# Kernel optimization log

Measured on AMD Instinct MI355X. Metric: run time of the kernel, lower is better.

The kernel has to match this reference:

```python
import jax, jax.numpy as jnp
import numpy as np

DIM = 1024
NUM_HEADS = 16
HEAD_DIM = 64
EPS = 1e-6

def setup_inputs() -> dict:
    key = jax.random.key(0)
    ks = jax.random.split(key, 6)
    x = jax.random.normal(ks[0], (4, 2048, DIM), dtype=jnp.float32)
    # Linear weights stored as (in, out); torch nn.Linear computes x @ W.T with W (out,in),
    # equivalent math with our (in,out) layout.
    Wq = jax.random.normal(ks[1], (DIM, NUM_HEADS * HEAD_DIM), dtype=jnp.float32) / np.sqrt(DIM)
    Wk = jax.random.normal(ks[2], (DIM, NUM_HEADS * HEAD_DIM), dtype=jnp.float32) / np.sqrt(DIM)
    Wv = jax.random.normal(ks[3], (DIM, NUM_HEADS * HEAD_DIM), dtype=jnp.float32) / np.sqrt(DIM)
    Wo = jax.random.normal(ks[4], (NUM_HEADS * HEAD_DIM, DIM), dtype=jnp.float32) / np.sqrt(NUM_HEADS * HEAD_DIM)
    # FeatureMap buffer: randn(head_dim, head_dim)/sqrt(head_dim)
    proj = jax.random.normal(ks[5], (HEAD_DIM, HEAD_DIM), dtype=jnp.float32) / np.sqrt(HEAD_DIM)
    return {"x": x, "Wq": Wq, "Wk": Wk, "Wv": Wv, "Wo": Wo, "proj": proj}

def _feature_map(x, proj):
    # phi(x) = elu(x @ proj) + 1  (positive features)
    return jax.nn.elu(x @ proj) + 1.0

def reference(x, Wq, Wk, Wv, Wo, proj):
    B, S, _ = x.shape
    H, D = NUM_HEADS, HEAD_DIM
    q = (x @ Wq).reshape(B, S, H, D)
    k = (x @ Wk).reshape(B, S, H, D)
    v = (x @ Wv).reshape(B, S, H, D)
    q = _feature_map(q, proj)
    k = _feature_map(k, proj)
    # scan over time: carry kv_state (B,H,D,D) and k_state (B,H,D)
    q_t = jnp.moveaxis(q, 1, 0)  # (S,B,H,D)
    k_t = jnp.moveaxis(k, 1, 0)
    v_t = jnp.moveaxis(v, 1, 0)

    def step(carry, qkv):
        kv, ksum = carry
        qt, kt, vt = qkv  # each (B,H,D)
        kv = kv + kt[..., :, None] * vt[..., None, :]  # outer product k v^T
        ksum = ksum + kt
        num = jnp.einsum('bhd,bhde->bhe', qt, kv)
        den = jnp.einsum('bhd,bhd->bh', qt, ksum) + EPS
        return (kv, ksum), num / den[..., None]

    kv0 = jnp.zeros((B, H, D, D), dtype=x.dtype)
    ks0 = jnp.zeros((B, H, D), dtype=x.dtype)
    _, out = jax.lax.scan(step, (kv0, ks0), (q_t, k_t, v_t))
    out = jnp.moveaxis(out, 0, 1).reshape(B, S, H * D)  # (B,S,H*D)
    return out @ Wo
```

## Files before the change

### kernel.cpp

```cpp
#include <hip/hip_runtime.h>

typedef unsigned short u16;
typedef unsigned int   u32;
typedef short bfrag8 __attribute__((ext_vector_type(8)));
typedef float facc4  __attribute__((ext_vector_type(4)));

#define DIM    1024
#define NH     16
#define HD     64
#define BSZ    4
#define SEQ    2048
#define MROWS  (BSZ*SEQ)
#define CHUNK  64
#define NCHUNK (SEQ/CHUNK)
#define BH     (BSZ*NH)
#define TS     72
#define NT     16

__device__ __forceinline__ u16 f2bf(float f) {
  u32 u = __builtin_bit_cast(u32, f);
  u32 r = u + 0x7fffu + ((u >> 16) & 1u);
  return (u16)(r >> 16);
}
__device__ __forceinline__ float bf2f(u16 b) {
  return __builtin_bit_cast(float, (u32)b << 16);
}

__device__ __forceinline__ void gload_lds16(const void* g, void* l) {
  __builtin_amdgcn_global_load_lds((const __attribute__((address_space(1))) u32*)g,
                                   (__attribute__((address_space(3))) u32*)l, 16, 0, 0);
}


__global__ __launch_bounds__(256) void conv_f32_bf16(const float* __restrict__ in, u16* __restrict__ out) {
  const int i = (blockIdx.x * 256 + threadIdx.x) * 4;
  const float4 v = *(const float4*)(in + i);
  ushort4 o;
  o.x = f2bf(v.x); o.y = f2bf(v.y); o.z = f2bf(v.z); o.w = f2bf(v.w);
  *(ushort4*)(out + i) = o;
}

__global__ __launch_bounds__(256) void fold_qk(const float* __restrict__ Wq, const float* __restrict__ Wk,
                                               const float* __restrict__ proj, u16* __restrict__ wt) {
  const int i0 = blockIdx.x * 32;
  const int h  = blockIdx.y;
  const int sel = blockIdx.z;
  const float* W = sel ? Wk : Wq;
  u16* out = wt + (size_t)sel * (DIM*DIM);
  __shared__ float sp[64*64];
  __shared__ float sw[32*64];
  const int tid = threadIdx.x;
  for (int idx = tid; idx < 4096; idx += 256) sp[idx] = proj[idx];
  for (int idx = tid; idx < 2048; idx += 256) {
    int r = idx >> 6, c = idx & 63;
    sw[idx] = W[(size_t)(i0 + r)*DIM + h*64 + c];
  }
  __syncthreads();
  const int i  = tid >> 3;
  const int e0 = (tid & 7) * 8;
  #pragma unroll
  for (int ee = 0; ee < 8; ++ee) {
    const int e = e0 + ee;
    float acc = 0.f;
    for (int d = 0; d < 64; ++d) acc += sw[i*64 + d] * sp[d*64 + e];
    out[(size_t)(h*64 + e)*DIM + i0 + i] = f2bf(acc);
  }
}

__global__ __launch_bounds__(256) void trans_conv(const float* __restrict__ Wv, const float* __restrict__ Wo,
                                                  u16* __restrict__ wt) {
  const int sel = blockIdx.z;
  const float* in = sel ? Wo : Wv;
  u16* out = wt + (size_t)(2 + sel) * (DIM*DIM);
  const int n0 = blockIdx.x * 32, k0 = blockIdx.y * 32;
  __shared__ float tile[32][33];
  const int tid = threadIdx.x;
  for (int idx = tid; idx < 1024; idx += 256) {
    int r = idx >> 5, c = idx & 31;
    tile[r][c] = in[(size_t)(k0 + r)*DIM + n0 + c];
  }
  __syncthreads();
  for (int idx = tid; idx < 1024; idx += 256) {
    int r = idx >> 5, c = idx & 31;
    out[(size_t)(n0 + r)*DIM + k0 + c] = f2bf(tile[c][r]);
  }
}


#define SBAR0() __builtin_amdgcn_sched_barrier(0)

#define STAGE6(kt, bp) { \
  const int rih = tid >> 3, sl = tid & 7; \
  const int gc = ((sl ^ (rih & 7)) << 3); \
  _Pragma("unroll") for (int seg = 0; seg < 2; ++seg) \
    gload_lds16(A + (size_t)(m0 + seg*64 + rih)*DIM + (kt)*64 + gc, (bp) + seg*4096 + tid*8); \
  _Pragma("unroll") for (int seg = 0; seg < 4; ++seg) \
    gload_lds16(W + (size_t)(ngl + seg*64 + rih)*DIM + (kt)*64 + gc, (bp) + 8192 + seg*4096 + tid*8); \
}

#define RD8(xd, wd, bp, KH) { \
  _Pragma("unroll") for (int mf = 0; mf < 4; ++mf) { \
    const int row = wm*64 + mf*16 + lr; \
    xd[mf] = *(const bfrag8*)&(bp)[row*64 + ((((KH)*4+g) ^ (row & 7)) << 3)]; } \
  _Pragma("unroll") for (int nf = 0; nf < 4; ++nf) { \
    const int row = wn*64 + nf*16 + lr; \
    wd[nf] = *(const bfrag8*)&(bp)[8192 + row*64 + ((((KH)*4+g) ^ (row & 7)) << 3)]; } \
}

#define MM16(xs, ws) { __builtin_amdgcn_s_setprio(1); \
  _Pragma("unroll") for (int nf = 0; nf < 4; ++nf) \
    _Pragma("unroll") for (int mf = 0; mf < 4; ++mf) \
      acc[nf][mf] = __builtin_amdgcn_mfma_f32_16x16x32_bf16(ws[nf], xs[mf], acc[nf][mf], 0, 0, 0); \
  __builtin_amdgcn_s_setprio(0); }

template<int MODE>
__global__ __launch_bounds__(512, 1)
void gemmK(const u16* __restrict__ A, const u16* __restrict__ W,
           u16* __restrict__ outb, float* __restrict__ outf) {
  __shared__ u16 lds[2*24576];
  const int tid  = threadIdx.x;
  const int wave = tid >> 6, lane = tid & 63;
  const int wm = wave >> 2, wn = wave & 3;
  const int lr = lane & 15, g = lane >> 4;

  const int NY  = (MODE == 0) ? 12 : 4;
  const int q   = (int)gridDim.x >> 3;
  const int bid = (int)blockIdx.x;
  const int nf_ = (bid & 7) * q + (bid >> 3);
  const int m0  = (nf_ / NY) * 128;
  const int ngl = (nf_ % NY) * 256;

  STAGE6(0, lds);
  STAGE6(1, lds + 24576);
  asm volatile("s_waitcnt vmcnt(6)" ::: "memory");
  asm volatile("s_barrier" ::: "memory");

  facc4 acc[4][4] = {};
  bfrag8 xa[4], wa[4], xb[4], wb[4];

  RD8(xa, wa, lds, 0);

  #pragma unroll 2
  for (int t = 0; t < NT; ++t) {
    u16* bufp = lds + (t & 1) * 24576;
    u16* bufq = lds + ((t + 1) & 1) * 24576;
    asm volatile("s_waitcnt lgkmcnt(0)" ::: "memory"); SBAR0();
    RD8(xb, wb, bufp, 1);
    SBAR0();
    MM16(xa, wa);
    SBAR0();
    asm volatile("s_waitcnt vmcnt(0)" ::: "memory");
    asm volatile("s_barrier" ::: "memory");
    asm volatile("s_waitcnt lgkmcnt(0)" ::: "memory"); SBAR0();
    if (t + 2 < NT) STAGE6(t + 2, bufp);
    if (t + 1 < NT) RD8(xa, wa, bufq, 0);
    SBAR0();
    MM16(xb, wb);
    SBAR0();
    asm volatile("s_barrier" ::: "memory");
  }

  const int sel = (MODE == 0) ? (ngl >> 10) : 0;
  const bool doElu = (MODE == 0) && (sel < 2);
  const int coly = (MODE == 0) ? (ngl & 1023) : ngl;
  #pragma unroll
  for (int nf = 0; nf < 4; ++nf) {
    #pragma unroll
    for (int mf = 0; mf < 4; ++mf) {
      const facc4 a = acc[nf][mf];
      const int m = m0 + wm*64 + mf*16 + lr;
      const int col0 = coly + wn*64 + nf*16 + g*4;
      float v0 = a[0], v1 = a[1], v2 = a[2], v3 = a[3];
      if (MODE == 0) {
        if (doElu) {
          v0 = (v0 > 0.f) ? (v0 + 1.f) : __expf(v0);
          v1 = (v1 > 0.f) ? (v1 + 1.f) : __expf(v1);
          v2 = (v2 > 0.f) ? (v2 + 1.f) : __expf(v2);
          v3 = (v3 > 0.f) ? (v3 + 1.f) : __expf(v3);
        }
        uint2 pk;
        pk.x = (u32)f2bf(v0) | ((u32)f2bf(v1) << 16);
        pk.y = (u32)f2bf(v2) | ((u32)f2bf(v3) << 16);
        *(uint2*)&outb[(size_t)sel*((size_t)MROWS*DIM) + (size_t)m*DIM + col0] = pk;
      } else {
        float4 pk; pk.x = v0; pk.y = v1; pk.z = v2; pk.w = v3;
        *(float4*)&outf[(size_t)m*DIM + col0] = pk;
      }
    }
  }
}


__global__ __launch_bounds__(256) void phaseA(const u16* __restrict__ Kb, const u16* __restrict__ Vb,
                                              u16* __restrict__ Ast, float* __restrict__ ksum) {
  const int c = blockIdx.x, bh = blockIdx.y;
  const int b = bh >> 4, h = bh & 15;
  const int tid = threadIdx.x;
  const int wave = tid >> 6, lane = tid & 63, lr = lane & 15, g = lane >> 4;
  __shared__ u16 lKt[64*TS];
  __shared__ u16 lVt[64*TS];
  const size_t mbase = (size_t)b*SEQ + (size_t)c*CHUNK;

  for (int s = tid; s < 512; s += 256) {
    const int t = s >> 3, dg = (s & 7) * 8;
    const bfrag8 kk = *(const bfrag8*)&Kb[(mbase + t)*DIM + h*64 + dg];
    const bfrag8 vv = *(const bfrag8*)&Vb[(mbase + t)*DIM + h*64 + dg];
    #pragma unroll
    for (int j = 0; j < 8; ++j) {
      lKt[(dg + j)*TS + t] = (u16)kk[j];
      lVt[(dg + j)*TS + t] = (u16)vv[j];
    }
  }
  __syncthreads();

  facc4 acc[4] = {};
  #pragma unroll
  for (int kt = 0; kt < 2; ++kt) {
    const bfrag8 af = *(const bfrag8*)&lVt[(wave*16 + lr)*TS + kt*32 + g*8];
    #pragma unroll
    for (int j = 0; j < 4; ++j) {
      const bfrag8 bk = *(const bfrag8*)&lKt[(j*16 + lr)*TS + kt*32 + g*8];
      acc[j] = __builtin_amdgcn_mfma_f32_16x16x32_bf16(af, bk, acc[j], 0, 0, 0);
    }
  }
  u16* dst = Ast + (((size_t)bh*NCHUNK + c) << 12);
  #pragma unroll
  for (int j = 0; j < 4; ++j)
    #pragma unroll
    for (int r = 0; r < 4; ++r)
      dst[(wave*16 + g*4 + r)*64 + j*16 + lr] = f2bf(acc[j][r]);

  const int d = tid >> 2, seg = tid & 3;
  const bfrag8 k0 = *(const bfrag8*)&lKt[d*TS + seg*16];
  const bfrag8 k1 = *(const bfrag8*)&lKt[d*TS + seg*16 + 8];
  float s = 0.f;
  #pragma unroll
  for (int j = 0; j < 8; ++j) s += bf2f((u16)k0[j]) + bf2f((u16)k1[j]);
  s += __shfl_xor(s, 1, 64);
  s += __shfl_xor(s, 2, 64);
  if (seg == 0) ksum[((size_t)bh*NCHUNK + c)*64 + d] = s;
}

__global__ __launch_bounds__(256) void phaseB(u16* __restrict__ Ast, float* __restrict__ ksum) {
  const int bh = blockIdx.x, slice = blockIdx.y;
  const int tid = threadIdx.x;
  u16* base = Ast + (size_t)bh*NCHUNK*4096 + slice*256 + tid;
  float v[NCHUNK];
  #pragma unroll
  for (int c = 0; c < NCHUNK; ++c) v[c] = bf2f(base[(size_t)c*4096]);
  float run = 0.f;
  #pragma unroll
  for (int c = 0; c < NCHUNK; ++c) { base[(size_t)c*4096] = f2bf(run); run += v[c]; }
  if (slice == 0 && tid < 64) {
    float rs = 0.f;
    float* kp = ksum + (size_t)bh*NCHUNK*64 + tid;
    for (int c = 0; c < NCHUNK; ++c) { const float t = kp[c*64]; kp[c*64] = rs; rs += t; }
  }
}

__global__ __launch_bounds__(256) void phaseC(const u16* __restrict__ Qb, const u16* __restrict__ Kb,
                                              const u16* __restrict__ Vb, const u16* __restrict__ Ast,
                                              const float* __restrict__ ksum, u16* __restrict__ Ob) {
  const int c = blockIdx.x, bh = blockIdx.y;
  const int b = bh >> 4, h = bh & 15;
  const int tid = threadIdx.x;
  const int wave = tid >> 6, lane = tid & 63, lr = lane & 15, g = lane >> 4;
  __shared__ u16 lS  [64*TS];
  __shared__ u16 lVt [64*TS];
  __shared__ u16 lKVt[64*TS];
  __shared__ float lks[64];
  __shared__ float lrs[64];
  __shared__ float lqk[64];
  const size_t mbase = (size_t)b*SEQ + (size_t)c*CHUNK;

  for (int s = tid; s < 512; s += 256) {
    const int t = s >> 3, dg = (s & 7) * 8;
    const bfrag8 vv = *(const bfrag8*)&Vb[(mbase + t)*DIM + h*64 + dg];
    #pragma unroll
    for (int j = 0; j < 8; ++j) lVt[(dg + j)*TS + t] = (u16)vv[j];
  }
  const u16* kvsrc = Ast + (((size_t)bh*NCHUNK + c) << 12);
  for (int s = tid; s < 512; s += 256) {
    const int e = s >> 3, dg = (s & 7) * 8;
    *(bfrag8*)&lKVt[e*TS + dg] = *(const bfrag8*)&kvsrc[e*64 + dg];
  }
  if (tid < 64) lks[tid] = ksum[((size_t)bh*NCHUNK + c)*64 + tid];

  bfrag8 qf[2], kf[4][2];
  {
    const u16* qrow = Qb + (mbase + wave*16 + lr)*DIM + h*64;
    qf[0] = *(const bfrag8*)&qrow[g*8];
    qf[1] = *(const bfrag8*)&qrow[32 + g*8];
  }
  #pragma unroll
  for (int j = 0; j < 4; ++j) {
    const u16* krow = Kb + (mbase + j*16 + lr)*DIM + h*64;
    kf[j][0] = *(const bfrag8*)&krow[g*8];
    kf[j][1] = *(const bfrag8*)&krow[32 + g*8];
  }

  facc4 accs[4] = {};
  #pragma unroll
  for (int kt = 0; kt < 2; ++kt)
    #pragma unroll
    for (int j = 0; j < 4; ++j)
      accs[j] = __builtin_amdgcn_mfma_f32_16x16x32_bf16(qf[kt], kf[j][kt], accs[j], 0, 0, 0);

  float rs[4] = {0.f, 0.f, 0.f, 0.f};
  #pragma unroll
  for (int j = 0; j < 4; ++j) {
    const int cc = j*16 + lr;
    #pragma unroll
    for (int r = 0; r < 4; ++r) {
      const int rr = wave*16 + g*4 + r;
      const float vS = (cc <= rr) ? accs[j][r] : 0.f;
      rs[r] += vS;
      lS[rr*TS + cc] = f2bf(vS);
    }
  }
  #pragma unroll
  for (int r = 0; r < 4; ++r) {
    float t = rs[r];
    t += __shfl_xor(t, 1, 64); t += __shfl_xor(t, 2, 64);
    t += __shfl_xor(t, 4, 64); t += __shfl_xor(t, 8, 64);
    if (lr == 0) lrs[wave*16 + g*4 + r] = t;
  }
  __syncthreads();

  {
    const u16* qr2 = Qb + (mbase + wave*16 + lr)*DIM + h*64 + g*16;
    const bfrag8 a0 = *(const bfrag8*)&qr2[0];
    const bfrag8 a1 = *(const bfrag8*)&qr2[8];
    float t = 0.f;
    #pragma unroll
    for (int j = 0; j < 8; ++j)
      t += bf2f((u16)a0[j]) * lks[g*16 + j] + bf2f((u16)a1[j]) * lks[g*16 + 8 + j];
    t += __shfl_xor(t, 16, 64);
    t += __shfl_xor(t, 32, 64);
    if (g == 0) lqk[wave*16 + lr] = t;
  }

  facc4 acco[4] = {};
  #pragma unroll
  for (int kt = 0; kt < 2; ++kt) {
    const bfrag8 sf = *(const bfrag8*)&lS[(wave*16 + lr)*TS + kt*32 + g*8];
    #pragma unroll
    for (int j = 0; j < 4; ++j) {
      const bfrag8 vf = *(const bfrag8*)&lVt[(j*16 + lr)*TS + kt*32 + g*8];
      acco[j] = __builtin_amdgcn_mfma_f32_16x16x32_bf16(sf, vf, acco[j], 0, 0, 0);
    }
  }
  #pragma unroll
  for (int kt = 0; kt < 2; ++kt)
    #pragma unroll
    for (int j = 0; j < 4; ++j) {
      const bfrag8 kvf = *(const bfrag8*)&lKVt[(j*16 + lr)*TS + kt*32 + g*8];
      acco[j] = __builtin_amdgcn_mfma_f32_16x16x32_bf16(qf[kt], kvf, acco[j], 0, 0, 0);
    }

  #pragma unroll
  for (int r = 0; r < 4; ++r) {
    const int rr = wave*16 + g*4 + r;
    const float rden = 1.0f / (lrs[rr] + lqk[rr] + 1e-6f);
    #pragma unroll
    for (int j = 0; j < 4; ++j)
      Ob[(mbase + rr)*DIM + h*64 + j*16 + lr] = f2bf(acco[j][r] * rden);
  }
}

extern "C" void kernel_launch(void* const* d_in, const int* in_sizes, int n_in,
                              void* d_out, int out_size, void* d_ws, size_t ws_size,
                              hipStream_t stream) {
  const float* x    = (const float*)d_in[0];
  const float* Wq   = (const float*)d_in[1];
  const float* Wk   = (const float*)d_in[2];
  const float* Wv   = (const float*)d_in[3];
  const float* Wo   = (const float*)d_in[4];
  const float* proj = (const float*)d_in[5];
  float* out = (float*)d_out;

  char* ws = (char*)d_ws;
  u16*   xb   = (u16*)  (ws);
  u16*   wt   = (u16*)  (ws + 16777216);
  u16*   qkv  = (u16*)  (ws + 25165824);
  u16*   Ob   = (u16*)  (ws + 75497472);
  u16*   Ast  = (u16*)  (ws + 92274688);
  float* ksum = (float*)(ws + 109051904);
  (void)ws_size; (void)in_sizes; (void)n_in; (void)out_size;

  conv_f32_bf16<<<dim3((MROWS*DIM)/1024), 256, 0, stream>>>(x, xb);
  fold_qk      <<<dim3(DIM/32, NH, 2), 256, 0, stream>>>(Wq, Wk, proj, wt);
  trans_conv   <<<dim3(DIM/32, DIM/32, 2), 256, 0, stream>>>(Wv, Wo, wt);

  gemmK<0><<<dim3(64*12), 512, 0, stream>>>(xb, wt, qkv, nullptr);

  const u16* Qb = qkv;
  const u16* Kb = qkv + (size_t)MROWS*DIM;
  const u16* Vb = qkv + 2*(size_t)MROWS*DIM;

  phaseA<<<dim3(NCHUNK, BH), 256, 0, stream>>>(Kb, Vb, Ast, ksum);
  phaseB<<<dim3(BH, 16), 256, 0, stream>>>(Ast, ksum);
  phaseC<<<dim3(NCHUNK, BH), 256, 0, stream>>>(Qb, Kb, Vb, Ast, ksum, Ob);

  gemmK<1><<<dim3(64*4), 512, 0, stream>>>(Ob, wt + 3*(size_t)DIM*DIM, nullptr, out);
}
```

Baseline: 186.6 us.

## Merge prep kernels and fold chunk prefix sum into phaseC

```diff
diff --git a/kernel.cpp b/kernel.cpp
--- a/kernel.cpp
+++ b/kernel.cpp
@@ -31,61 +31,62 @@
                                    (__attribute__((address_space(3))) u32*)l, 16, 0, 0);
 }
 
-
-__global__ __launch_bounds__(256) void conv_f32_bf16(const float* __restrict__ in, u16* __restrict__ out) {
-  const int i = (blockIdx.x * 256 + threadIdx.x) * 4;
-  const float4 v = *(const float4*)(in + i);
-  ushort4 o;
-  o.x = f2bf(v.x); o.y = f2bf(v.y); o.z = f2bf(v.z); o.w = f2bf(v.w);
-  *(ushort4*)(out + i) = o;
-}
-
-__global__ __launch_bounds__(256) void fold_qk(const float* __restrict__ Wq, const float* __restrict__ Wk,
-                                               const float* __restrict__ proj, u16* __restrict__ wt) {
-  const int i0 = blockIdx.x * 32;
-  const int h  = blockIdx.y;
-  const int sel = blockIdx.z;
-  const float* W = sel ? Wk : Wq;
-  u16* out = wt + (size_t)sel * (DIM*DIM);
-  __shared__ float sp[64*64];
-  __shared__ float sw[32*64];
-  const int tid = threadIdx.x;
-  for (int idx = tid; idx < 4096; idx += 256) sp[idx] = proj[idx];
-  for (int idx = tid; idx < 2048; idx += 256) {
-    int r = idx >> 6, c = idx & 63;
-    sw[idx] = W[(size_t)(i0 + r)*DIM + h*64 + c];
-  }
-  __syncthreads();
-  const int i  = tid >> 3;
-  const int e0 = (tid & 7) * 8;
-  #pragma unroll
-  for (int ee = 0; ee < 8; ++ee) {
-    const int e = e0 + ee;
-    float acc = 0.f;
-    for (int d = 0; d < 64; ++d) acc += sw[i*64 + d] * sp[d*64 + e];
-    out[(size_t)(h*64 + e)*DIM + i0 + i] = f2bf(acc);
-  }
-}
-
-__global__ __launch_bounds__(256) void trans_conv(const float* __restrict__ Wv, const float* __restrict__ Wo,
-                                                  u16* __restrict__ wt) {
-  const int sel = blockIdx.z;
-  const float* in = sel ? Wo : Wv;
-  u16* out = wt + (size_t)(2 + sel) * (DIM*DIM);
-  const int n0 = blockIdx.x * 32, k0 = blockIdx.y * 32;
-  __shared__ float tile[32][33];
-  const int tid = threadIdx.x;
-  for (int idx = tid; idx < 1024; idx += 256) {
-    int r = idx >> 5, c = idx & 31;
-    tile[r][c] = in[(size_t)(k0 + r)*DIM + n0 + c];
-  }
-  __syncthreads();
-  for (int idx = tid; idx < 1024; idx += 256) {
-    int r = idx >> 5, c = idx & 31;
-    out[(size_t)(n0 + r)*DIM + k0 + c] = f2bf(tile[c][r]);
-  }
-}
-
+__global__ __launch_bounds__(256) void prep(const float* __restrict__ x,
+                                            const float* __restrict__ Wq, const float* __restrict__ Wk,
+                                            const float* __restrict__ Wv, const float* __restrict__ Wo,
+                                            const float* __restrict__ proj,
+                                            u16* __restrict__ xb, u16* __restrict__ wt) {
+  __shared__ float smem[6144];
+  const int bx = blockIdx.x, tid = threadIdx.x;
+  if (bx < 8192) {
+    const int i = (bx * 256 + tid) * 4;
+    const float4 v = *(const float4*)(x + i);
+    ushort4 o;
+    o.x = f2bf(v.x); o.y = f2bf(v.y); o.z = f2bf(v.z); o.w = f2bf(v.w);
+    *(ushort4*)(xb + i) = o;
+  } else if (bx < 9216) {
+    const int idx = bx - 8192;
+    const int i0 = (idx & 31) * 32;
+    const int h  = (idx >> 5) & 15;
+    const int sel = idx >> 9;
+    const float* W = sel ? Wk : Wq;
+    u16* out = wt + (size_t)sel * (DIM*DIM);
+    float* sp = smem;
+    float* sw = smem + 4096;
+    for (int s = tid; s < 4096; s += 256) sp[s] = proj[s];
+    for (int s = tid; s < 2048; s += 256) {
+      int r = s >> 6, c = s & 63;
+      sw[s] = W[(size_t)(i0 + r)*DIM + h*64 + c];
+    }
+    __syncthreads();
+    const int i  = tid >> 3;
+    const int e0 = (tid & 7) * 8;
+    #pragma unroll
+    for (int ee = 0; ee < 8; ++ee) {
+      const int e = e0 + ee;
+      float acc = 0.f;
+      for (int d = 0; d < 64; ++d) acc += sw[i*64 + d] * sp[d*64 + e];
+      out[(size_t)(h*64 + e)*DIM + i0 + i] = f2bf(acc);
+    }
+  } else {
+    const int idx = bx - 9216;
+    const int n0 = (idx & 31) * 32;
+    const int k0 = ((idx >> 5) & 31) * 32;
+    const int sel = idx >> 10;
+    const float* in = sel ? Wo : Wv;
+    u16* out = wt + (size_t)(2 + sel) * (DIM*DIM);
+    float* tile = smem;
+    for (int s = tid; s < 1024; s += 256) {
+      int r = s >> 5, c = s & 31;
+      tile[r*33 + c] = in[(size_t)(k0 + r)*DIM + n0 + c];
+    }
+    __syncthreads();
+    for (int s = tid; s < 1024; s += 256) {
+      int r = s >> 5, c = s & 31;
+      out[(size_t)(n0 + r)*DIM + k0 + c] = f2bf(tile[c*33 + r]);
+    }
+  }
+}
 
 #define SBAR0() __builtin_amdgcn_sched_barrier(0)
 
@@ -241,23 +242,6 @@
   if (seg == 0) ksum[((size_t)bh*NCHUNK + c)*64 + d] = s;
 }
 
-__global__ __launch_bounds__(256) void phaseB(u16* __restrict__ Ast, float* __restrict__ ksum) {
-  const int bh = blockIdx.x, slice = blockIdx.y;
-  const int tid = threadIdx.x;
-  u16* base = Ast + (size_t)bh*NCHUNK*4096 + slice*256 + tid;
-  float v[NCHUNK];
-  #pragma unroll
-  for (int c = 0; c < NCHUNK; ++c) v[c] = bf2f(base[(size_t)c*4096]);
-  float run = 0.f;
-  #pragma unroll
-  for (int c = 0; c < NCHUNK; ++c) { base[(size_t)c*4096] = f2bf(run); run += v[c]; }
-  if (slice == 0 && tid < 64) {
-    float rs = 0.f;
-    float* kp = ksum + (size_t)bh*NCHUNK*64 + tid;
-    for (int c = 0; c < NCHUNK; ++c) { const float t = kp[c*64]; kp[c*64] = rs; rs += t; }
-  }
-}
-
 __global__ __launch_bounds__(256) void phaseC(const u16* __restrict__ Qb, const u16* __restrict__ Kb,
                                               const u16* __restrict__ Vb, const u16* __restrict__ Ast,
                                               const float* __restrict__ ksum, u16* __restrict__ Ob) {
@@ -279,12 +263,28 @@
     #pragma unroll
     for (int j = 0; j < 8; ++j) lVt[(dg + j)*TS + t] = (u16)vv[j];
   }
-  const u16* kvsrc = Ast + (((size_t)bh*NCHUNK + c) << 12);
-  for (int s = tid; s < 512; s += 256) {
-    const int e = s >> 3, dg = (s & 7) * 8;
-    *(bfrag8*)&lKVt[e*TS + dg] = *(const bfrag8*)&kvsrc[e*64 + dg];
-  }
-  if (tid < 64) lks[tid] = ksum[((size_t)bh*NCHUNK + c)*64 + tid];
+  {
+    float pacc[16] = {};
+    const u16* abase = Ast + (((size_t)bh*NCHUNK) << 12) + tid*16;
+    for (int cc = 0; cc < c; ++cc) {
+      const bfrag8 a0 = *(const bfrag8*)&abase[(size_t)cc*4096];
+      const bfrag8 a1 = *(const bfrag8*)&abase[(size_t)cc*4096 + 8];
+      #pragma unroll
+      for (int jj = 0; jj < 8; ++jj) {
+        pacc[jj]     += bf2f((u16)a0[jj]);
+        pacc[8 + jj] += bf2f((u16)a1[jj]);
+      }
+    }
+    const int e = tid >> 2, d0 = (tid & 3) * 16;
+    #pragma unroll
+    for (int jj = 0; jj < 16; ++jj) lKVt[e*TS + d0 + jj] = f2bf(pacc[jj]);
+  }
+  if (tid < 64) {
+    float s = 0.f;
+    const float* kb = ksum + (size_t)bh*NCHUNK*64 + tid;
+    for (int cc = 0; cc < c; ++cc) s += kb[(size_t)cc*64];
+    lks[tid] = s;
+  }
 
   bfrag8 qf[2], kf[4][2];
   {
@@ -388,9 +388,7 @@
   float* ksum = (float*)(ws + 109051904);
   (void)ws_size; (void)in_sizes; (void)n_in; (void)out_size;
 
-  conv_f32_bf16<<<dim3((MROWS*DIM)/1024), 256, 0, stream>>>(x, xb);
-  fold_qk      <<<dim3(DIM/32, NH, 2), 256, 0, stream>>>(Wq, Wk, proj, wt);
-  trans_conv   <<<dim3(DIM/32, DIM/32, 2), 256, 0, stream>>>(Wv, Wo, wt);
+  prep<<<dim3(11264), 256, 0, stream>>>(x, Wq, Wk, Wv, Wo, proj, xb, wt);
 
   gemmK<0><<<dim3(64*12), 512, 0, stream>>>(xb, wt, qkv, nullptr);
 
@@ -399,7 +397,6 @@
   const u16* Vb = qkv + 2*(size_t)MROWS*DIM;
 
   phaseA<<<dim3(NCHUNK, BH), 256, 0, stream>>>(Kb, Vb, Ast, ksum);
-  phaseB<<<dim3(BH, 16), 256, 0, stream>>>(Ast, ksum);
   phaseC<<<dim3(NCHUNK, BH), 256, 0, stream>>>(Qb, Kb, Vb, Ast, ksum, Ob);
 
   gemmK<1><<<dim3(64*4), 512, 0, stream>>>(Ob, wt + 3*(size_t)DIM*DIM, nullptr, out);
```

New measurement: 213.0 us. +14.1%, slower.
